# Optimization experiments

Measured on AMD Instinct MI355X. Metric: run time of the kernel, lower is better.

Reference implementation:

```python
import jax, jax.numpy as jnp
import numpy as np

N = 100000
E = 3200000
EPS = 1e-5


def setup_inputs() -> dict:
    key = jax.random.key(0)
    ks = jax.random.split(key, 6)
    x = jax.random.normal(ks[0], (N, 512), dtype=jnp.float32)
    edge_row = jax.random.randint(ks[1], (E,), 0, N, dtype=jnp.int32)
    edge_col = jax.random.randint(ks[2], (E,), 0, N, dtype=jnp.int32)
    edge_val = jax.random.uniform(ks[3], (E,), dtype=jnp.float32)
    W1 = jax.random.normal(ks[4], (512, 256), dtype=jnp.float32) * (1.0 / np.sqrt(512))
    W2 = jax.random.normal(ks[5], (256, 64), dtype=jnp.float32) * (1.0 / np.sqrt(256))
    gamma1 = jnp.ones((256,), jnp.float32)
    beta1 = jnp.zeros((256,), jnp.float32)
    gamma2 = jnp.ones((64,), jnp.float32)
    beta2 = jnp.zeros((64,), jnp.float32)
    return dict(x=x, edge_row=edge_row, edge_col=edge_col, edge_val=edge_val,
                W1=W1, gamma1=gamma1, beta1=beta1, W2=W2, gamma2=gamma2, beta2=beta2)


def spmm(row, col, val, dense):
    # out[i] = sum_{e: row[e]==i} val[e] * dense[col[e]]
    msgs = val[:, None] * dense[col]  # [E, F]
    return jax.ops.segment_sum(msgs, row, num_segments=N)


def batchnorm(h, gamma, beta):
    # BatchNorm1d in training mode: batch (node-dim) statistics, biased variance
    mean = jnp.mean(h, axis=0)
    var = jnp.var(h, axis=0)
    return (h - mean) * jax.lax.rsqrt(var + EPS) * gamma + beta


def reference(x, edge_row, edge_col, edge_val, W1, gamma1, beta1, W2, gamma2, beta2):
    # layer 1: dense GEMM -> sparse aggregate -> relu (GNNLayer active=True)
    h = spmm(edge_row, edge_col, edge_val, x @ W1)
    h = jax.nn.relu(h)
    h = batchnorm(h, gamma1, beta1)
    h = jax.nn.relu(h)
    # dropout treated as identity (inference mode) for deterministic reference
    h = spmm(edge_row, edge_col, edge_val, h @ W2)
    h = jax.nn.relu(h)
    h = batchnorm(h, gamma2, beta2)
    return h
```

## Files before the change

### kernel.cpp

```cpp
#include <hip/hip_runtime.h>

#define EPS 1e-5f

typedef __attribute__((ext_vector_type(8))) short short8;
typedef __attribute__((ext_vector_type(4))) float floatx4;
typedef __attribute__((ext_vector_type(4))) unsigned short ushortx4;
typedef __attribute__((ext_vector_type(2))) unsigned short ushortx2;

__device__ __forceinline__ unsigned short f2bf(float f) {
    unsigned u = __float_as_uint(f);
    unsigned r = (u + 0x7FFFu + ((u >> 16) & 1u)) >> 16;
    return (unsigned short)r;
}
__device__ __forceinline__ float bf2f(unsigned short h) {
    return __uint_as_float((unsigned)h << 16);
}

__global__ void zero_kernel(int* __restrict__ counts, float* __restrict__ stats,
                            int n_counts, int n_stats) {
    int i = blockIdx.x * 256 + threadIdx.x;
    if (i < n_counts) counts[i] = 0;
    if (i < n_stats)  stats[i] = 0.0f;
}

__global__ __launch_bounds__(256) void count_kernel(const int* __restrict__ erow,
                                                    int* __restrict__ counts, int E) {
    int stride = gridDim.x * 256;
    for (int j = blockIdx.x * 256 + threadIdx.x; j < E; j += stride)
        atomicAdd(&counts[erow[j]], 1);
}

__global__ __launch_bounds__(1024) void row_scan_kernel(const int* __restrict__ counts,
                                                        int* __restrict__ row_start,
                                                        int* __restrict__ bucket_cursor,
                                                        int n, int E) {
    __shared__ int lds[1024];
    int t = threadIdx.x;
    int per = (n + 1023) >> 10;
    int s0 = t * per, s1 = min(s0 + per, n);
    int sum = 0;
    for (int i = s0; i < s1; i++) sum += counts[i];
    lds[t] = sum;
    __syncthreads();
    for (int off = 1; off < 1024; off <<= 1) {
        int v = (t >= off) ? lds[t - off] : 0;
        __syncthreads();
        lds[t] += v;
        __syncthreads();
    }
    int run = lds[t] - sum;
    for (int i = s0; i < s1; i++) {
        row_start[i] = run;
        if ((i & 127) == 0) bucket_cursor[(i >> 7) * 16] = run;
        run += counts[i];
    }
    if (t == 0) row_start[n] = E;
}

__global__ __launch_bounds__(256) void bucket_scatter_kernel(const int* __restrict__ erow,
                                                             const int* __restrict__ ecol,
                                                             const float* __restrict__ ev,
                                                             int* __restrict__ bucket_cursor,
                                                             int2* __restrict__ tmp, int E) {
    int stride = gridDim.x * 256;
    for (int j = blockIdx.x * 256 + threadIdx.x; j < E; j += stride) {
        int r = erow[j];
        int b = r >> 7, lr = r & 127;
        int p = atomicAdd(&bucket_cursor[b * 16], 1);
        tmp[p] = make_int2(ecol[j] | (lr << 17), __float_as_int(ev[j]));
    }
}

__global__ __launch_bounds__(256) void place_kernel(const int2* __restrict__ tmp,
                                                    const int* __restrict__ row_start,
                                                    int2* __restrict__ edges,
                                                    int n, int E) {
    __shared__ int cur[128];
    int b = blockIdx.x, t = threadIdx.x;
    int rbase = b << 7;
    int rend  = min(rbase + 128, n);
    int bstart = row_start[rbase];
    int bend   = row_start[rend];
    if (t < 128) {
        int r = rbase + t;
        cur[t] = (r < n) ? row_start[r] : E;
    }
    __syncthreads();
    for (int j = bstart + t; j < bend; j += 256) {
        int2 e = tmp[j];
        int lr = ((unsigned)e.x) >> 17;
        int pos = atomicAdd(&cur[lr], 1);
        edges[pos] = make_int2(e.x & 0x1FFFF, e.y);
    }
}

__global__ void prep_w1_kernel(const float* __restrict__ W1,
                               unsigned short* __restrict__ Bhi,
                               unsigned short* __restrict__ Blo) {
    int idx = blockIdx.x * 256 + threadIdx.x;
    int nn = idx >> 9, k = idx & 511;
    float w = W1[(size_t)k * 256 + nn];
    unsigned short hi = f2bf(w);
    float rem = w - bf2f(hi);
    Bhi[idx] = hi;
    Blo[idx] = f2bf(rem);
}

__global__ __launch_bounds__(256) void gemm1_mfma_kernel(const float* __restrict__ A,
                                                         const unsigned short* __restrict__ Bhi,
                                                         const unsigned short* __restrict__ Blo,
                                                         unsigned short* __restrict__ H0, int M) {
    __shared__ unsigned short AsH[128][32];
    __shared__ unsigned short AsL[128][32];
    __shared__ unsigned short BsH[128][32];
    __shared__ unsigned short BsL[128][32];
    int tid  = threadIdx.x;
    int lane = tid & 63, w = tid >> 6;
    int wm = w & 1, wn = w >> 1;
    int rowBase = blockIdx.y * 128;
    int colBase = blockIdx.x * 128;

    floatx4 acc[4][4];
#pragma unroll
    for (int i = 0; i < 4; i++)
#pragma unroll
        for (int j = 0; j < 4; j++)
#pragma unroll
            for (int r = 0; r < 4; r++) acc[i][j][r] = 0.0f;

    int r    = tid >> 1;
    int half = tid & 1;
    bool aval = (rowBase + r) < M;
    const float* aptr = A + (size_t)(rowBase + r) * 512 + half * 16;
    const unsigned short* bhptr = Bhi + (size_t)(colBase + r) * 512 + half * 16;
    const unsigned short* blptr = Blo + (size_t)(colBase + r) * 512 + half * 16;

    int cl = lane & 15, quad = lane >> 4;
    int q8 = quad * 8;

    for (int k0 = 0; k0 < 512; k0 += 32) {
        float f[16];
        if (aval) {
            *(float4*)&f[0]  = *(const float4*)(aptr + k0);
            *(float4*)&f[4]  = *(const float4*)(aptr + k0 + 4);
            *(float4*)&f[8]  = *(const float4*)(aptr + k0 + 8);
            *(float4*)&f[12] = *(const float4*)(aptr + k0 + 12);
        } else {
#pragma unroll
            for (int t = 0; t < 16; t++) f[t] = 0.0f;
        }
        union { unsigned short s[16]; uint4 q[2]; } ph, pl;
#pragma unroll
        for (int t = 0; t < 16; t++) {
            unsigned short hi = f2bf(f[t]);
            ph.s[t] = hi;
            pl.s[t] = f2bf(f[t] - bf2f(hi));
        }
        *(uint4*)&AsH[r][half * 16]     = ph.q[0];
        *(uint4*)&AsH[r][half * 16 + 8] = ph.q[1];
        *(uint4*)&AsL[r][half * 16]     = pl.q[0];
        *(uint4*)&AsL[r][half * 16 + 8] = pl.q[1];
        *(uint4*)&BsH[r][half * 16]     = *(const uint4*)(bhptr + k0);
        *(uint4*)&BsH[r][half * 16 + 8] = *(const uint4*)(bhptr + k0 + 8);
        *(uint4*)&BsL[r][half * 16]     = *(const uint4*)(blptr + k0);
        *(uint4*)&BsL[r][half * 16 + 8] = *(const uint4*)(blptr + k0 + 8);
        __syncthreads();

        short8 ah[4], al[4], bh[4], bl[4];
#pragma unroll
        for (int mt = 0; mt < 4; mt++) {
            ah[mt] = *(short8*)&AsH[wm * 64 + mt * 16 + cl][q8];
            al[mt] = *(short8*)&AsL[wm * 64 + mt * 16 + cl][q8];
        }
#pragma unroll
        for (int nt = 0; nt < 4; nt++) {
            bh[nt] = *(short8*)&BsH[wn * 64 + nt * 16 + cl][q8];
            bl[nt] = *(short8*)&BsL[wn * 64 + nt * 16 + cl][q8];
        }
#pragma unroll
        for (int mt = 0; mt < 4; mt++)
#pragma unroll
            for (int nt = 0; nt < 4; nt++) {
                acc[mt][nt] = __builtin_amdgcn_mfma_f32_16x16x32_bf16(ah[mt], bh[nt], acc[mt][nt], 0, 0, 0);
                acc[mt][nt] = __builtin_amdgcn_mfma_f32_16x16x32_bf16(al[mt], bh[nt], acc[mt][nt], 0, 0, 0);
                acc[mt][nt] = __builtin_amdgcn_mfma_f32_16x16x32_bf16(ah[mt], bl[nt], acc[mt][nt], 0, 0, 0);
            }
        __syncthreads();
    }

#pragma unroll
    for (int mt = 0; mt < 4; mt++) {
#pragma unroll
        for (int reg = 0; reg < 4; reg++) {
            int gr = rowBase + wm * 64 + mt * 16 + quad * 4 + reg;
            if (gr < M) {
#pragma unroll
                for (int nt = 0; nt < 4; nt++) {
                    H0[(size_t)gr * 256 + colBase + wn * 64 + nt * 16 + cl] = f2bf(acc[mt][nt][reg]);
                }
            }
        }
    }
}

__global__ __launch_bounds__(256) void agg1_kernel(const unsigned short* __restrict__ H0,
                                                   const int* __restrict__ rs,
                                                   const int2* __restrict__ edges,
                                                   float* __restrict__ H1, int n) {
    int g = threadIdx.x >> 5, sub = threadIdx.x & 31;
    int i = blockIdx.x * 8 + g;
    if (i >= n) return;
    int start = rs[i], end = rs[i + 1];
    int fo = blockIdx.y * 128 + (sub << 2);
    float accx = 0.f, accy = 0.f, accz = 0.f, accw = 0.f;
    int j = start;
    for (; j + 8 <= end; j += 8) {
        int2 e[8];
        ushortx4 u[8];
#pragma unroll
        for (int t = 0; t < 8; t++) e[t] = edges[j + t];
#pragma unroll
        for (int t = 0; t < 8; t++)
            u[t] = *(const ushortx4*)(H0 + (size_t)e[t].x * 256 + fo);
#pragma unroll
        for (int t = 0; t < 8; t++) {
            float v = __int_as_float(e[t].y);
            accx += v * bf2f(u[t].x);
            accy += v * bf2f(u[t].y);
            accz += v * bf2f(u[t].z);
            accw += v * bf2f(u[t].w);
        }
    }
    for (; j < end; j++) {
        int2 e = edges[j];
        float v = __int_as_float(e.y);
        ushortx4 u = *(const ushortx4*)(H0 + (size_t)e.x * 256 + fo);
        accx += v * bf2f(u.x);
        accy += v * bf2f(u.y);
        accz += v * bf2f(u.z);
        accw += v * bf2f(u.w);
    }
    float4 o;
    o.x = fmaxf(accx, 0.f); o.y = fmaxf(accy, 0.f);
    o.z = fmaxf(accz, 0.f); o.w = fmaxf(accw, 0.f);
    *(float4*)(H1 + (size_t)i * 256 + fo) = o;
}

__global__ __launch_bounds__(256) void colstats1_kernel(const float* __restrict__ H1,
                                                        float* __restrict__ sums,
                                                        float* __restrict__ sumsq,
                                                        int n, int rpb) {
    int tid = threadIdx.x;
    int r0 = blockIdx.x * rpb;
    int r1 = min(r0 + rpb, n);
    float s = 0.f, q = 0.f;
    for (int rr = r0; rr < r1; rr++) {
        float v = H1[(size_t)rr * 256 + tid];
        s += v; q += v * v;
    }
    atomicAdd(&sums[tid], s);
    atomicAdd(&sumsq[tid], q);
}

__global__ void bnparams_kernel(const float* __restrict__ sums, const float* __restrict__ sumsq,
                                const float* __restrict__ gamma, const float* __restrict__ beta,
                                float* __restrict__ scale, float* __restrict__ shift,
                                int C, float invN) {
    int c = threadIdx.x;
    if (c < C) {
        float mean = sums[c] * invN;
        float var  = sumsq[c] * invN - mean * mean;
        float rstd = rsqrtf(var + EPS);
        float sc   = gamma[c] * rstd;
        scale[c] = sc;
        shift[c] = beta[c] - mean * sc;
    }
}

__global__ __launch_bounds__(256) void gemm2_kernel(const float* __restrict__ H1,
                                                    const float* __restrict__ W2,
                                                    const float* __restrict__ scale1,
                                                    const float* __restrict__ shift1,
                                                    unsigned short* __restrict__ H2, int M) {
    __shared__ float As[8][129];
    __shared__ float Bs[8][64];
    int tid = threadIdx.x;
    int tx = tid & 15, ty = tid >> 4;
    int rowBase = blockIdx.x * 128;
    float acc[8][4];
#pragma unroll
    for (int i = 0; i < 8; i++)
#pragma unroll
        for (int j = 0; j < 4; j++) acc[i][j] = 0.0f;

    int r   = tid >> 1;
    int kq  = (tid & 1) * 4;
    int bkk = tid >> 6;
    int bcol = tid & 63;

    for (int k0 = 0; k0 < 256; k0 += 8) {
        float4 a4 = make_float4(0.f, 0.f, 0.f, 0.f);
        int arow = rowBase + r;
        if (arow < M) a4 = *(const float4*)(H1 + (size_t)arow * 256 + k0 + kq);
        float av[4] = {a4.x, a4.y, a4.z, a4.w};
#pragma unroll
        for (int jj = 0; jj < 4; jj++) {
            int kk = k0 + kq + jj;
            float t = av[jj] * scale1[kk] + shift1[kk];
            As[kq + jj][r] = fmaxf(t, 0.0f);
        }
        Bs[bkk][bcol]     = W2[(size_t)(k0 + bkk) * 64 + bcol];
        Bs[bkk + 4][bcol] = W2[(size_t)(k0 + bkk + 4) * 64 + bcol];
        __syncthreads();
#pragma unroll
        for (int k = 0; k < 8; k++) {
            float ra[8], rb[4];
#pragma unroll
            for (int i = 0; i < 8; i++) ra[i] = As[k][ty * 8 + i];
#pragma unroll
            for (int j = 0; j < 4; j++) rb[j] = Bs[k][tx * 4 + j];
#pragma unroll
            for (int i = 0; i < 8; i++)
#pragma unroll
                for (int j = 0; j < 4; j++) acc[i][j] += ra[i] * rb[j];
        }
        __syncthreads();
    }
#pragma unroll
    for (int i = 0; i < 8; i++) {
        int crow = rowBase + ty * 8 + i;
        if (crow < M) {
            ushortx4 o;
            o.x = f2bf(acc[i][0]); o.y = f2bf(acc[i][1]);
            o.z = f2bf(acc[i][2]); o.w = f2bf(acc[i][3]);
            *(ushortx4*)(H2 + (size_t)crow * 64 + tx * 4) = o;
        }
    }
}

__global__ __launch_bounds__(256) void agg2_kernel(const unsigned short* __restrict__ H2,
                                                   const int* __restrict__ rs,
                                                   const int2* __restrict__ edges,
                                                   float* __restrict__ H3, int n) {
    int w = threadIdx.x >> 6, lane = threadIdx.x & 63;
    int half = lane >> 5, sub = lane & 31;
    int i = blockIdx.x * 8 + w * 2 + half;
    if (i >= n) return;
    int start = rs[i], end = rs[i + 1];
    int fo = sub << 1;
    float accx = 0.f, accy = 0.f;
    int j = start;
    for (; j + 4 <= end; j += 4) {
        int2 e[4];
        ushortx2 u[4];
#pragma unroll
        for (int t = 0; t < 4; t++) e[t] = edges[j + t];
#pragma unroll
        for (int t = 0; t < 4; t++)
            u[t] = *(const ushortx2*)(H2 + (size_t)e[t].x * 64 + fo);
#pragma unroll
        for (int t = 0; t < 4; t++) {
            float v = __int_as_float(e[t].y);
            accx += v * bf2f(u[t].x);
            accy += v * bf2f(u[t].y);
        }
    }
    for (; j < end; j++) {
        int2 e = edges[j];
        float v = __int_as_float(e.y);
        ushortx2 u = *(const ushortx2*)(H2 + (size_t)e.x * 64 + fo);
        accx += v * bf2f(u.x);
        accy += v * bf2f(u.y);
    }
    float2 o;
    o.x = fmaxf(accx, 0.f);
    o.y = fmaxf(accy, 0.f);
    *(float2*)(H3 + (size_t)i * 64 + fo) = o;
}

__global__ __launch_bounds__(256) void colstats2_kernel(const float* __restrict__ H3,
                                                        float* __restrict__ sums,
                                                        float* __restrict__ sumsq,
                                                        int n, int rpb) {
    int c = threadIdx.x & 63, rsub = threadIdx.x >> 6;
    int base = blockIdx.x * rpb;
    int r1 = min(base + rpb, n);
    float s = 0.f, q = 0.f;
    for (int rr = base + rsub; rr < r1; rr += 4) {
        float v = H3[(size_t)rr * 64 + c];
        s += v; q += v * v;
    }
    atomicAdd(&sums[c], s);
    atomicAdd(&sumsq[c], q);
}

__global__ void bnapply_kernel(float* __restrict__ out, const float* __restrict__ scale,
                               const float* __restrict__ shift, int total) {
    int idx = blockIdx.x * 256 + threadIdx.x;
    if (idx < total) {
        int c = idx & 63;
        out[idx] = out[idx] * scale[c] + shift[c];
    }
}

extern "C" void kernel_launch(void* const* d_in, const int* in_sizes, int n_in,
                              void* d_out, int out_size, void* d_ws, size_t ws_size,
                              hipStream_t stream) {
    const float* x    = (const float*)d_in[0];
    const int*   erow = (const int*)d_in[1];
    const int*   ecol = (const int*)d_in[2];
    const float* ev   = (const float*)d_in[3];
    const float* W1   = (const float*)d_in[4];
    const float* g1   = (const float*)d_in[5];
    const float* b1   = (const float*)d_in[6];
    const float* W2   = (const float*)d_in[7];
    const float* g2   = (const float*)d_in[8];
    const float* b2   = (const float*)d_in[9];
    float* out = (float*)d_out;

    int n = in_sizes[0] / 512;
    int E = in_sizes[1];
    int nb = (n + 127) >> 7;

    char* ws = (char*)d_ws;
    size_t off = 0;
    auto alloc = [&](size_t bytes) { size_t o = off; off += (bytes + 255) & ~(size_t)255; return o; };

    int*   row_counts    = (int*)(ws + alloc((size_t)n * 4));
    int*   row_start     = (int*)(ws + alloc((size_t)(n + 1) * 4));
    int*   bucket_cursor = (int*)(ws + alloc((size_t)nb * 16 * 4));
    int2*  tmp           = (int2*)(ws + alloc((size_t)E * 8));
    int2*  edges         = (int2*)(ws + alloc((size_t)E * 8));
    unsigned short* h0  = (unsigned short*)(ws + alloc((size_t)n * 256 * 2));
    float* h1           = (float*)(ws + alloc((size_t)n * 256 * 4));
    unsigned short* h2  = (unsigned short*)(ws + alloc((size_t)n * 64 * 2));
    unsigned short* w1hi = (unsigned short*)(ws + alloc((size_t)256 * 512 * 2));
    unsigned short* w1lo = (unsigned short*)(ws + alloc((size_t)256 * 512 * 2));
    float* stats        = (float*)(ws + alloc(2048 * 4));
    float* sums1  = stats;
    float* sumsq1 = stats + 256;
    float* sums2  = stats + 512;
    float* sumsq2 = stats + 576;
    float* scale1 = stats + 640;
    float* shift1 = stats + 896;
    float* scale2 = stats + 1152;
    float* shift2 = stats + 1216;

    float invN = 1.0f / (float)n;

    zero_kernel<<<dim3((n + 255) / 256), dim3(256), 0, stream>>>(row_counts, stats, n, 640);
    count_kernel<<<dim3(2048), dim3(256), 0, stream>>>(erow, row_counts, E);
    row_scan_kernel<<<dim3(1), dim3(1024), 0, stream>>>(row_counts, row_start, bucket_cursor, n, E);
    bucket_scatter_kernel<<<dim3(2048), dim3(256), 0, stream>>>(erow, ecol, ev, bucket_cursor, tmp, E);
    place_kernel<<<dim3(nb), dim3(256), 0, stream>>>(tmp, row_start, edges, n, E);
    prep_w1_kernel<<<dim3(512), dim3(256), 0, stream>>>(W1, w1hi, w1lo);
    gemm1_mfma_kernel<<<dim3(2, (n + 127) / 128), dim3(256), 0, stream>>>(x, w1hi, w1lo, h0, n);
    agg1_kernel<<<dim3((n + 7) / 8, 2), dim3(256), 0, stream>>>(h0, row_start, edges, h1, n);
    colstats1_kernel<<<dim3(400), dim3(256), 0, stream>>>(h1, sums1, sumsq1, n, (n + 399) / 400);
    bnparams_kernel<<<dim3(1), dim3(256), 0, stream>>>(sums1, sumsq1, g1, b1, scale1, shift1, 256, invN);
    gemm2_kernel<<<dim3((n + 127) / 128), dim3(256), 0, stream>>>(h1, W2, scale1, shift1, h2, n);
    agg2_kernel<<<dim3((n + 7) / 8), dim3(256), 0, stream>>>(h2, row_start, edges, out, n);
    colstats2_kernel<<<dim3(200), dim3(256), 0, stream>>>(out, sums2, sumsq2, n, (n + 199) / 200);
    bnparams_kernel<<<dim3(1), dim3(64), 0, stream>>>(sums2, sumsq2, g2, b2, scale2, shift2, 64, invN);
    bnapply_kernel<<<dim3((n * 64 + 255) / 256), dim3(256), 0, stream>>>(out, scale2, shift2, n * 64);

    (void)n_in; (void)out_size; (void)ws_size;
}
```

Before: 1.355 ms.

## Build CSR via per-bucket LDS histograms instead of per-row global counts

Replaces the per-row global atomic count and the single-block 100k-element serial scan with an LDS-privatized bucket histogram and a small scan over buckets. Row offsets are now computed inside place_kernel by a per-bucket local count and prefix scan over the bucketed edges. This removes millions of global atomics and a long serial scan, but adds an extra read pass over tmp and assumes at most 1024 buckets.

```diff
diff --git a/kernel.cpp b/kernel.cpp
--- a/kernel.cpp
+++ b/kernel.cpp
@@ -16,45 +16,51 @@
     return __uint_as_float((unsigned)h << 16);
 }
 
-__global__ void zero_kernel(int* __restrict__ counts, float* __restrict__ stats,
-                            int n_counts, int n_stats) {
+__global__ void zero_kernel(int* __restrict__ hist, float* __restrict__ stats,
+                            int nb, int n_stats) {
     int i = blockIdx.x * 256 + threadIdx.x;
-    if (i < n_counts) counts[i] = 0;
-    if (i < n_stats)  stats[i] = 0.0f;
-}
-
-__global__ __launch_bounds__(256) void count_kernel(const int* __restrict__ erow,
-                                                    int* __restrict__ counts, int E) {
+    if (i < nb)      hist[i] = 0;
+    if (i < n_stats) stats[i] = 0.0f;
+}
+
+__global__ __launch_bounds__(256) void bucket_hist_kernel(const int* __restrict__ erow,
+                                                          int* __restrict__ hist,
+                                                          int E, int nb) {
+    __shared__ int cnt[1024];
+    for (int i = threadIdx.x; i < nb; i += 256) cnt[i] = 0;
+    __syncthreads();
     int stride = gridDim.x * 256;
     for (int j = blockIdx.x * 256 + threadIdx.x; j < E; j += stride)
-        atomicAdd(&counts[erow[j]], 1);
-}
-
-__global__ __launch_bounds__(1024) void row_scan_kernel(const int* __restrict__ counts,
-                                                        int* __restrict__ row_start,
-                                                        int* __restrict__ bucket_cursor,
-                                                        int n, int E) {
+        atomicAdd(&cnt[erow[j] >> 7], 1);
+    __syncthreads();
+    for (int i = threadIdx.x; i < nb; i += 256) {
+        int c = cnt[i];
+        if (c) atomicAdd(&hist[i], c);
+    }
+}
+
+__global__ __launch_bounds__(1024) void bucket_scan_kernel(const int* __restrict__ hist,
+                                                           int* __restrict__ bucket_start,
+                                                           int* __restrict__ bucket_cursor,
+                                                           int* __restrict__ row_start,
+                                                           int nb, int n, int E) {
     __shared__ int lds[1024];
     int t = threadIdx.x;
-    int per = (n + 1023) >> 10;
-    int s0 = t * per, s1 = min(s0 + per, n);
-    int sum = 0;
-    for (int i = s0; i < s1; i++) sum += counts[i];
-    lds[t] = sum;
+    int v = (t < nb) ? hist[t] : 0;
+    lds[t] = v;
     __syncthreads();
     for (int off = 1; off < 1024; off <<= 1) {
-        int v = (t >= off) ? lds[t - off] : 0;
-        __syncthreads();
-        lds[t] += v;
-        __syncthreads();
-    }
-    int run = lds[t] - sum;
-    for (int i = s0; i < s1; i++) {
-        row_start[i] = run;
-        if ((i & 127) == 0) bucket_cursor[(i >> 7) * 16] = run;
-        run += counts[i];
-    }
-    if (t == 0) row_start[n] = E;
+        int w = (t >= off) ? lds[t - off] : 0;
+        __syncthreads();
+        lds[t] += w;
+        __syncthreads();
+    }
+    int ex = lds[t] - v;
+    if (t < nb) {
+        bucket_start[t] = ex;
+        bucket_cursor[t * 16] = ex;
+    }
+    if (t == 0) { bucket_start[nb] = E; row_start[n] = E; }
 }
 
 __global__ __launch_bounds__(256) void bucket_scatter_kernel(const int* __restrict__ erow,
@@ -72,18 +78,32 @@
 }
 
 __global__ __launch_bounds__(256) void place_kernel(const int2* __restrict__ tmp,
-                                                    const int* __restrict__ row_start,
-                                                    int2* __restrict__ edges,
-                                                    int n, int E) {
-    __shared__ int cur[128];
+                                                    const int* __restrict__ bucket_start,
+                                                    int* __restrict__ row_start,
+                                                    int2* __restrict__ edges, int n) {
+    __shared__ int cnt[128], scn[128], cur[128];
     int b = blockIdx.x, t = threadIdx.x;
-    int rbase = b << 7;
-    int rend  = min(rbase + 128, n);
-    int bstart = row_start[rbase];
-    int bend   = row_start[rend];
+    int bstart = bucket_start[b], bend = bucket_start[b + 1];
+    if (t < 128) cnt[t] = 0;
+    __syncthreads();
+    for (int j = bstart + t; j < bend; j += 256)
+        atomicAdd(&cnt[((unsigned)tmp[j].x) >> 17], 1);
+    __syncthreads();
+    if (t < 128) scn[t] = cnt[t];
+    __syncthreads();
+#pragma unroll
+    for (int off = 1; off < 128; off <<= 1) {
+        int v = 0;
+        if (t < 128 && t >= off) v = scn[t - off];
+        __syncthreads();
+        if (t < 128) scn[t] += v;
+        __syncthreads();
+    }
     if (t < 128) {
-        int r = rbase + t;
-        cur[t] = (r < n) ? row_start[r] : E;
+        int pref = bstart + scn[t] - cnt[t];
+        cur[t] = pref;
+        int r = b * 128 + t;
+        if (r < n) row_start[r] = pref;
     }
     __syncthreads();
     for (int j = bstart + t; j < bend; j += 256) {
@@ -426,9 +446,10 @@
     size_t off = 0;
     auto alloc = [&](size_t bytes) { size_t o = off; off += (bytes + 255) & ~(size_t)255; return o; };
 
-    int*   row_counts    = (int*)(ws + alloc((size_t)n * 4));
+    int*   hist          = (int*)(ws + alloc((size_t)nb * 4));
+    int*   bucket_start  = (int*)(ws + alloc((size_t)(nb + 1) * 4));
+    int*   bucket_cursor = (int*)(ws + alloc((size_t)nb * 16 * 4));
     int*   row_start     = (int*)(ws + alloc((size_t)(n + 1) * 4));
-    int*   bucket_cursor = (int*)(ws + alloc((size_t)nb * 16 * 4));
     int2*  tmp           = (int2*)(ws + alloc((size_t)E * 8));
     int2*  edges         = (int2*)(ws + alloc((size_t)E * 8));
     unsigned short* h0  = (unsigned short*)(ws + alloc((size_t)n * 256 * 2));
@@ -448,11 +469,11 @@
 
     float invN = 1.0f / (float)n;
 
-    zero_kernel<<<dim3((n + 255) / 256), dim3(256), 0, stream>>>(row_counts, stats, n, 640);
-    count_kernel<<<dim3(2048), dim3(256), 0, stream>>>(erow, row_counts, E);
-    row_scan_kernel<<<dim3(1), dim3(1024), 0, stream>>>(row_counts, row_start, bucket_cursor, n, E);
+    zero_kernel<<<dim3((nb + 255) / 256), dim3(256), 0, stream>>>(hist, stats, nb, 640);
+    bucket_hist_kernel<<<dim3(1024), dim3(256), 0, stream>>>(erow, hist, E, nb);
+    bucket_scan_kernel<<<dim3(1), dim3(1024), 0, stream>>>(hist, bucket_start, bucket_cursor, row_start, nb, n, E);
     bucket_scatter_kernel<<<dim3(2048), dim3(256), 0, stream>>>(erow, ecol, ev, bucket_cursor, tmp, E);
-    place_kernel<<<dim3(nb), dim3(256), 0, stream>>>(tmp, row_start, edges, n, E);
+    place_kernel<<<dim3(nb), dim3(256), 0, stream>>>(tmp, bucket_start, row_start, edges, n);
     prep_w1_kernel<<<dim3(512), dim3(256), 0, stream>>>(W1, w1hi, w1lo);
     gemm1_mfma_kernel<<<dim3(2, (n + 127) / 128), dim3(256), 0, stream>>>(x, w1hi, w1lo, h0, n);
     agg1_kernel<<<dim3((n + 7) / 8, 2), dim3(256), 0, stream>>>(h0, row_start, edges, h1, n);
```

After: 1.105 ms. 18.5% less time.
